# Performance work log

Measured on AMD Instinct MI355X. Metric: run time of the kernel, lower is better.

The kernel has to match this reference:

```python
import jax, jax.numpy as jnp
import numpy as np

P_DROP = 0.6  # dropout prob from the source module
N_NODES = 50000
N_EDGES = 800000


def _cheb_edge_weights(edge_index, num_nodes):
    # ChebConv with sym normalization and default lambda_max=2.0:
    # scaled Laplacian hat(L) = 2L/lambda_max - I = -D^{-1/2} A D^{-1/2}
    # (diagonal becomes 0), so edge weight = -1/sqrt(deg[row]*deg[col]).
    row, col = edge_index[0], edge_index[1]
    deg = jnp.zeros((num_nodes,), jnp.float32).at[row].add(1.0)
    dis = jnp.where(deg > 0, jax.lax.rsqrt(jnp.maximum(deg, 1.0)), 0.0)
    return -dis[row] * dis[col]


def _prop(x, row, col, w, n):
    # hat(L) @ x via gather-scale-scatter over the edge list
    return jnp.zeros((n, x.shape[1]), x.dtype).at[row].add(w[:, None] * x[col])


def _cheb_conv(x, row, col, w, W, b, n):
    # Chebyshev recursion: Tx0 = x, Tx1 = hat(L) x, Tx_k = 2 hat(L) Tx_{k-1} - Tx_{k-2}
    Tx0 = x
    out = Tx0 @ W[0]
    Tx1 = _prop(Tx0, row, col, w, n)
    out = out + Tx1 @ W[1]
    for k in range(2, W.shape[0]):
        Tx2 = 2.0 * _prop(Tx1, row, col, w, n) - Tx0
        out = out + Tx2 @ W[k]
        Tx0, Tx1 = Tx1, Tx2
    return out + b


def _dropout(x, key, p):
    keep = jax.random.bernoulli(key, 1.0 - p, x.shape)
    return jnp.where(keep, x * (1.0 / (1.0 - p)), 0.0)


def setup_inputs() -> dict:
    key = jax.random.key(0)
    ks = jax.random.split(key, 8)
    x = jax.random.normal(ks[0], (N_NODES, 64), jnp.float32)
    edge_index = jax.random.randint(ks[1], (2, N_EDGES), 0, N_NODES, jnp.int64)
    W0 = jax.random.normal(ks[2], (2, 64, 64), jnp.float32) * 0.1
    b0 = jnp.zeros((64,), jnp.float32)
    W1 = jax.random.normal(ks[3], (2, 64, 64), jnp.float32) * 0.1
    b1 = jnp.zeros((64,), jnp.float32)
    W2 = jax.random.normal(ks[4], (2, 64, 32), jnp.float32) * 0.1
    b2 = jnp.zeros((32,), jnp.float32)
    return {"x": x, "edge_index": edge_index, "W0": W0, "b0": b0,
            "W1": W1, "b1": b1, "W2": W2, "b2": b2}


def reference(x, edge_index, W0, b0, W1, b1, W2, b2):
    row, col = edge_index[0], edge_index[1]
    n = x.shape[0]
    w = _cheb_edge_weights(edge_index, n)
    dkey = jax.random.key(1)
    params = [(W0, b0), (W1, b1), (W2, b2)]
    for i, (W, b) in enumerate(params):
        x = _dropout(x, jax.random.fold_in(dkey, i), P_DROP)
        x = _cheb_conv(x, row, col, w, W, b, n)
        if i < len(params) - 1:
            x = jax.nn.relu(x)
    return x
```

## Files before the change

### kernel.cpp

```cpp
#include <hip/hip_runtime.h>
#include <stdint.h>

typedef _Float16 half8 __attribute__((ext_vector_type(8)));
typedef float float4v __attribute__((ext_vector_type(4)));

__host__ __device__ inline void tf2x32(uint32_t k0, uint32_t k1,
                                       uint32_t x0, uint32_t x1,
                                       uint32_t* o0, uint32_t* o1) {
  const uint32_t ks2 = k0 ^ k1 ^ 0x1BD11BDAu;
#define ROTL(v, s) (((v) << (s)) | ((v) >> (32 - (s))))
#define RND(r) do { x0 += x1; x1 = ROTL(x1, r); x1 ^= x0; } while (0)
  x0 += k0; x1 += k1;
  RND(13); RND(15); RND(26); RND(6);
  x0 += k1; x1 += ks2 + 1u;
  RND(17); RND(29); RND(16); RND(24);
  x0 += ks2; x1 += k0 + 2u;
  RND(13); RND(15); RND(26); RND(6);
  x0 += k0; x1 += k1 + 3u;
  RND(17); RND(29); RND(16); RND(24);
  x0 += k1; x1 += ks2 + 4u;
  RND(13); RND(15); RND(26); RND(6);
  x0 += ks2; x1 += k0 + 5u;
  *o0 = x0; *o1 = x1;
#undef RND
#undef ROTL
}

__device__ inline bool drop_keep(uint32_t k0, uint32_t k1, uint32_t idx) {
  uint32_t o0, o1;
  tf2x32(k0, k1, 0u, idx, &o0, &o1);
  uint32_t bits = o0 ^ o1;
  float u = __uint_as_float((bits >> 9) | 0x3f800000u) - 1.0f;
  return u < 0.4f;
}

__global__ void k_fill2(const int* __restrict__ row, const int* __restrict__ col,
                        int* __restrict__ cnt, uint16_t* __restrict__ cs,
                        int e, int rows_per_xcd) {
  const int owner = blockIdx.x & 7;
  const int i = (blockIdx.x >> 3) * 256 + threadIdx.x;
  if (i < e) {
    int r = row[i];
    if (r / rows_per_xcd == owner) {
      int pos = atomicAdd(&cnt[r], 1);
      if (pos < 64) cs[(r << 6) + pos] = (uint16_t)col[i];
    }
  }
}

__global__ void k_drop(const float* __restrict__ x, const int* __restrict__ cnt,
                       uint16_t* __restrict__ cs, float* __restrict__ dis,
                       _Float16* __restrict__ y, _Float16* __restrict__ ys,
                       _Float16* __restrict__ ysb, uint32_t k0, uint32_t k1,
                       int n, int nd,
                       const float* __restrict__ W0, const float* __restrict__ W1,
                       const float* __restrict__ W2, _Float16* __restrict__ wh) {
  int i = blockIdx.x * 256 + threadIdx.x;
  if (i < 20480) {
    int d = i;
    if (d < 8192) {
      int o = d >> 7, k = d & 127;
      wh[d] = (_Float16)W0[k * 64 + o];
    } else if (d < 16384) {
      int d1 = d - 8192, o = d1 >> 7, k = d1 & 127;
      wh[d] = (_Float16)W1[k * 64 + o];
    } else {
      int d2 = d - 16384, o = d2 >> 7, k = d2 & 127;
      wh[d] = (_Float16)W2[k * 32 + o];
    }
  }
  if (i < 64) {
    ys[((size_t)n << 6) + i]  = (_Float16)0.f;
    ysb[((size_t)n << 6) + i] = (_Float16)0.f;
  }
  if (i < nd) {
    const int r = i >> 6;
    const int t = i & 63;
    const int d = cnt[r];
    const float dis_r = (d > 0) ? rsqrtf((float)d) : 0.0f;
    float v = drop_keep(k0, k1, (uint32_t)i) ? x[i] * 2.5f : 0.0f;
    y[i]  = (_Float16)v;
    ys[i] = (_Float16)(dis_r * v);
    if (t == 0) dis[r] = dis_r;
    const int cn = d < 64 ? d : 64;
    const int rnd = (cn + 7) & ~7;
    if (t >= cn && t < rnd) cs[(r << 6) + t] = (uint16_t)n;
  }
}

template<int T>
__device__ __forceinline__ void gatherT(int idx_all, int rnd, int g, int sub,
                                        const _Float16* __restrict__ ysg,
                                        uint32_t dummy, float acc[8]) {
  half8 hv[T];
  #pragma unroll
  for (int j = 0; j < T; ++j) {
    int sh = __shfl(idx_all, j * 8 + g, 64);
    uint32_t c = (j * 8 < rnd) ? (uint32_t)(sh & 0xffff) : dummy;
    hv[j] = *(const half8*)((const char*)ysg + (c << 7) + (sub << 4));
  }
  #pragma unroll
  for (int j = 0; j < T; ++j)
    #pragma unroll
    for (int k = 0; k < 8; ++k) acc[k] += (float)hv[j][k];
}

template<int COUT, bool RELU, bool DROPN, bool WBF>
__global__ __launch_bounds__(256, 6) void k_conv(
    const _Float16* __restrict__ yg, const _Float16* __restrict__ ysg,
    const int* __restrict__ cnt, const uint16_t* __restrict__ cs,
    const float* __restrict__ dis, const _Float16* __restrict__ wt,
    const float* __restrict__ b, float* __restrict__ outf,
    _Float16* __restrict__ outb, _Float16* __restrict__ outs,
    uint32_t nk0, uint32_t nk1, int n) {
  constexpr int R  = 16;
  constexpr int TS = 136;
  __shared__ __align__(16) _Float16 xp[R][TS];

  const int wave = threadIdx.x >> 6;
  const int t    = threadIdx.x & 63;
  const int row0 = blockIdx.x * R;
  const int g    = t >> 3;
  const int sub  = t & 7;
  const uint32_t dummy = (uint32_t)n;

  int      idxs[4], ds4[4];
  float    dv4[4];
  _Float16 ygv[4];
  #pragma unroll
  for (int i = 0; i < 4; ++i) {
    int r = row0 + wave * 4 + i;
    r = r < n ? r : n - 1;
    idxs[i] = cs[(r << 6) + t];
    ds4[i]  = cnt[r];
    dv4[i]  = dis[r];
    ygv[i]  = yg[(uint32_t)(r << 6) + t];
  }

  #pragma unroll
  for (int i = 0; i < 4; ++i) {
    const int cn  = ds4[i] < 64 ? ds4[i] : 64;
    const int rnd = (cn + 7) & ~7;
    float acc[8] = {0.f, 0.f, 0.f, 0.f, 0.f, 0.f, 0.f, 0.f};
    if (rnd <= 16)      gatherT<2>(idxs[i], rnd, g, sub, ysg, dummy, acc);
    else if (rnd <= 32) gatherT<4>(idxs[i], rnd, g, sub, ysg, dummy, acc);
    else                gatherT<8>(idxs[i], rnd, g, sub, ysg, dummy, acc);

    const bool b0 = (g & 1), b1 = (g & 2), b2 = (g & 4);
    float a4[4], a2[2], v;
    #pragma unroll
    for (int m = 0; m < 4; ++m) {
      float keep = b0 ? acc[2 * m + 1] : acc[2 * m];
      float send = b0 ? acc[2 * m]     : acc[2 * m + 1];
      a4[m] = keep + __shfl_xor(send, 8, 64);
    }
    #pragma unroll
    for (int m = 0; m < 2; ++m) {
      float keep = b1 ? a4[2 * m + 1] : a4[2 * m];
      float send = b1 ? a4[2 * m]     : a4[2 * m + 1];
      a2[m] = keep + __shfl_xor(send, 16, 64);
    }
    {
      float keep = b2 ? a2[1] : a2[0];
      float send = b2 ? a2[0] : a2[1];
      v = keep + __shfl_xor(send, 32, 64);
    }
    const int rl = wave * 4 + i;
    xp[rl][t]                    = ygv[i];
    xp[rl][64 + (sub * 8 + g)]   = (_Float16)(-dv4[i] * v);
  }
  __syncthreads();

  constexpr int NW = COUT / 16;
  const int nn   = t & 15;
  const int quad = t >> 4;
  if (wave < NW) {
    const int colg = wave * 16 + nn;
    float4v acc = {0.f, 0.f, 0.f, 0.f};
    #pragma unroll
    for (int ks = 0; ks < 4; ++ks) {
      half8 a  = *(const half8*)&xp[nn][quad * 8 + 32 * ks];
      half8 bb = *(const half8*)&wt[(size_t)colg * 128 + quad * 8 + 32 * ks];
      acc = __builtin_amdgcn_mfma_f32_16x16x32_f16(a, bb, acc, 0, 0, 0);
    }
    const float bias = b[colg];
    #pragma unroll
    for (int rg = 0; rg < 4; ++rg) {
      const int rl = quad * 4 + rg;
      const int rr = row0 + rl;
      if (rr < n) {
        float v = acc[rg] + bias;
        if (RELU) v = fmaxf(v, 0.0f);
        if (DROPN) {
          if (drop_keep(nk0, nk1, (uint32_t)(rr * 64 + colg))) v *= 2.5f;
          else v = 0.0f;
        }
        if (WBF) {
          outb[(size_t)rr * COUT + colg] = (_Float16)v;
          outs[(size_t)rr * COUT + colg] = (_Float16)(dis[rr] * v);
        } else {
          outf[(size_t)rr * COUT + colg] = v;
        }
      }
    }
  }
}

extern "C" void kernel_launch(void* const* d_in, const int* in_sizes, int n_in,
                              void* d_out, int out_size, void* d_ws, size_t ws_size,
                              hipStream_t stream) {
  const float* x   = (const float*)d_in[0];
  const int*   ei  = (const int*)d_in[1];
  const float* W0  = (const float*)d_in[2];
  const float* b0  = (const float*)d_in[3];
  const float* W1f = (const float*)d_in[4];
  const float* b1  = (const float*)d_in[5];
  const float* W2  = (const float*)d_in[6];
  const float* b2  = (const float*)d_in[7];
  float* out = (float*)d_out;

  const int n = in_sizes[0] / 64;
  const int e = in_sizes[1] / 2;
  const int* row = ei;
  const int* col = ei + e;

  size_t off = 0;
  auto carve = [&](size_t elems) {
    size_t o = off;
    off += (elems + 255) & ~(size_t)255;
    return o;
  };
  int* base = (int*)d_ws;
  int*      cnt = base + carve(n);
  float*    dis = (float*)(base + carve(n));
  uint16_t* cs  = (uint16_t*)(base + carve((size_t)n * 32));
  _Float16* ya  = (_Float16*)(base + carve((size_t)n * 32));
  _Float16* ysa = (_Float16*)(base + carve((size_t)(n + 1) * 32));
  _Float16* yb  = (_Float16*)(base + carve((size_t)n * 32));
  _Float16* ysb = (_Float16*)(base + carve((size_t)(n + 1) * 32));
  _Float16* wh  = (_Float16*)(base + carve(10240));
  (void)ws_size;
  _Float16* wh0 = wh;
  _Float16* wh1 = wh + 8192;
  _Float16* wh2 = wh + 16384;

  uint32_t dk[3][2];
  for (uint32_t i = 0; i < 3; ++i) tf2x32(0u, 1u, 0u, i, &dk[i][0], &dk[i][1]);

  hipMemsetAsync(cnt, 0, (size_t)n * 4, stream);

  const int nchunk = (e + 255) / 256;
  const int bd = ((n * 64) + 255) / 256;
  const int bc = (n + 15) / 16;
  const int rpx = (n + 7) / 8;

  k_fill2<<<nchunk * 8, 256, 0, stream>>>(row, col, cnt, cs, e, rpx);
  k_drop<<<bd, 256, 0, stream>>>(x, cnt, cs, dis, ya, ysa, ysb,
                                 dk[0][0], dk[0][1], n, n * 64,
                                 W0, W1f, W2, wh);

  k_conv<64, true,  true,  true ><<<bc, 256, 0, stream>>>(
      ya, ysa, cnt, cs, dis, wh0, b0, nullptr, yb, ysb, dk[1][0], dk[1][1], n);
  k_conv<64, true,  true,  true ><<<bc, 256, 0, stream>>>(
      yb, ysb, cnt, cs, dis, wh1, b1, nullptr, ya, ysa, dk[2][0], dk[2][1], n);
  k_conv<32, false, false, false><<<bc, 256, 0, stream>>>(
      ya, ysa, cnt, cs, dis, wh2, b2, out, nullptr, nullptr, 0u, 0u, n);
}
```

Baseline: 188.7 us.

## Split scaled features into two 32-wide halves and vectorize edge fill loads

New measurement: 203.7 us. 7.9% more time.

```diff
diff --git a/kernel.cpp b/kernel.cpp
--- a/kernel.cpp
+++ b/kernel.cpp
@@ -38,21 +38,27 @@
                         int* __restrict__ cnt, uint16_t* __restrict__ cs,
                         int e, int rows_per_xcd) {
   const int owner = blockIdx.x & 7;
-  const int i = (blockIdx.x >> 3) * 256 + threadIdx.x;
-  if (i < e) {
-    int r = row[i];
-    if (r / rows_per_xcd == owner) {
-      int pos = atomicAdd(&cnt[r], 1);
-      if (pos < 64) cs[(r << 6) + pos] = (uint16_t)col[i];
+  const int i2 = (((blockIdx.x >> 3) * 256) + threadIdx.x) * 2;
+  if (i2 < e) {
+    const int2 r2 = *(const int2*)&row[i2];
+    const int2 c2 = *(const int2*)&col[i2];
+    if (r2.x / rows_per_xcd == owner) {
+      int pos = atomicAdd(&cnt[r2.x], 1);
+      if (pos < 64) cs[(r2.x << 6) + pos] = (uint16_t)c2.x;
+    }
+    if (r2.y / rows_per_xcd == owner) {
+      int pos = atomicAdd(&cnt[r2.y], 1);
+      if (pos < 64) cs[(r2.y << 6) + pos] = (uint16_t)c2.y;
     }
   }
 }
 
 __global__ void k_drop(const float* __restrict__ x, const int* __restrict__ cnt,
                        uint16_t* __restrict__ cs, float* __restrict__ dis,
-                       _Float16* __restrict__ y, _Float16* __restrict__ ys,
-                       _Float16* __restrict__ ysb, uint32_t k0, uint32_t k1,
-                       int n, int nd,
+                       _Float16* __restrict__ y,
+                       _Float16* __restrict__ ys0, _Float16* __restrict__ ys1,
+                       _Float16* __restrict__ ys0b, _Float16* __restrict__ ys1b,
+                       uint32_t k0, uint32_t k1, int n, int nd,
                        const float* __restrict__ W0, const float* __restrict__ W1,
                        const float* __restrict__ W2, _Float16* __restrict__ wh) {
   int i = blockIdx.x * 256 + threadIdx.x;
@@ -69,9 +75,10 @@
       wh[d] = (_Float16)W2[k * 32 + o];
     }
   }
-  if (i < 64) {
-    ys[((size_t)n << 6) + i]  = (_Float16)0.f;
-    ysb[((size_t)n << 6) + i] = (_Float16)0.f;
+  if (i < 32) {
+    const size_t dbase = (size_t)n * 32 + i;
+    ys0[dbase]  = (_Float16)0.f;  ys1[dbase]  = (_Float16)0.f;
+    ys0b[dbase] = (_Float16)0.f;  ys1b[dbase] = (_Float16)0.f;
   }
   if (i < nd) {
     const int r = i >> 6;
@@ -79,8 +86,10 @@
     const int d = cnt[r];
     const float dis_r = (d > 0) ? rsqrtf((float)d) : 0.0f;
     float v = drop_keep(k0, k1, (uint32_t)i) ? x[i] * 2.5f : 0.0f;
-    y[i]  = (_Float16)v;
-    ys[i] = (_Float16)(dis_r * v);
+    y[i] = (_Float16)v;
+    const _Float16 sv = (_Float16)(dis_r * v);
+    if (t < 32) ys0[(size_t)r * 32 + t]        = sv;
+    else        ys1[(size_t)r * 32 + (t - 32)] = sv;
     if (t == 0) dis[r] = dis_r;
     const int cn = d < 64 ? d : 64;
     const int rnd = (cn + 7) & ~7;
@@ -89,15 +98,15 @@
 }
 
 template<int T>
-__device__ __forceinline__ void gatherT(int idx_all, int rnd, int g, int sub,
-                                        const _Float16* __restrict__ ysg,
+__device__ __forceinline__ void gatherH(int idx_all, int rnd, int g2, int sub,
+                                        const _Float16* __restrict__ ysh,
                                         uint32_t dummy, float acc[8]) {
   half8 hv[T];
   #pragma unroll
   for (int j = 0; j < T; ++j) {
-    int sh = __shfl(idx_all, j * 8 + g, 64);
-    uint32_t c = (j * 8 < rnd) ? (uint32_t)(sh & 0xffff) : dummy;
-    hv[j] = *(const half8*)((const char*)ysg + (c << 7) + (sub << 4));
+    int sh = __shfl(idx_all, j * 16 + g2, 64);
+    uint32_t c = (j * 16 + g2 < rnd) ? (uint32_t)(sh & 0xffff) : dummy;
+    hv[j] = *(const half8*)((const char*)ysh + (c << 6) + (sub << 4));
   }
   #pragma unroll
   for (int j = 0; j < T; ++j)
@@ -107,11 +116,13 @@
 
 template<int COUT, bool RELU, bool DROPN, bool WBF>
 __global__ __launch_bounds__(256, 6) void k_conv(
-    const _Float16* __restrict__ yg, const _Float16* __restrict__ ysg,
+    const _Float16* __restrict__ yg,
+    const _Float16* __restrict__ ysg0, const _Float16* __restrict__ ysg1,
     const int* __restrict__ cnt, const uint16_t* __restrict__ cs,
     const float* __restrict__ dis, const _Float16* __restrict__ wt,
     const float* __restrict__ b, float* __restrict__ outf,
-    _Float16* __restrict__ outb, _Float16* __restrict__ outs,
+    _Float16* __restrict__ outb,
+    _Float16* __restrict__ outs0, _Float16* __restrict__ outs1,
     uint32_t nk0, uint32_t nk1, int n) {
   constexpr int R  = 16;
   constexpr int TS = 136;
@@ -120,11 +131,11 @@
   const int wave = threadIdx.x >> 6;
   const int t    = threadIdx.x & 63;
   const int row0 = blockIdx.x * R;
-  const int g    = t >> 3;
-  const int sub  = t & 7;
+  const int g2   = t >> 2;
+  const int sub  = t & 3;
   const uint32_t dummy = (uint32_t)n;
 
-  int      idxs[4], ds4[4];
+  int      idxs[4], rnd4[4];
   float    dv4[4];
   _Float16 ygv[4];
   #pragma unroll
@@ -132,43 +143,51 @@
     int r = row0 + wave * 4 + i;
     r = r < n ? r : n - 1;
     idxs[i] = cs[(r << 6) + t];
-    ds4[i]  = cnt[r];
+    const int d = cnt[r];
+    const int cn = d < 64 ? d : 64;
+    rnd4[i] = (cn + 7) & ~7;
     dv4[i]  = dis[r];
     ygv[i]  = yg[(uint32_t)(r << 6) + t];
   }
 
-  #pragma unroll
-  for (int i = 0; i < 4; ++i) {
-    const int cn  = ds4[i] < 64 ? ds4[i] : 64;
-    const int rnd = (cn + 7) & ~7;
-    float acc[8] = {0.f, 0.f, 0.f, 0.f, 0.f, 0.f, 0.f, 0.f};
-    if (rnd <= 16)      gatherT<2>(idxs[i], rnd, g, sub, ysg, dummy, acc);
-    else if (rnd <= 32) gatherT<4>(idxs[i], rnd, g, sub, ysg, dummy, acc);
-    else                gatherT<8>(idxs[i], rnd, g, sub, ysg, dummy, acc);
-
-    const bool b0 = (g & 1), b1 = (g & 2), b2 = (g & 4);
-    float a4[4], a2[2], v;
-    #pragma unroll
-    for (int m = 0; m < 4; ++m) {
-      float keep = b0 ? acc[2 * m + 1] : acc[2 * m];
-      float send = b0 ? acc[2 * m]     : acc[2 * m + 1];
-      a4[m] = keep + __shfl_xor(send, 8, 64);
-    }
-    #pragma unroll
-    for (int m = 0; m < 2; ++m) {
-      float keep = b1 ? a4[2 * m + 1] : a4[2 * m];
-      float send = b1 ? a4[2 * m]     : a4[2 * m + 1];
-      a2[m] = keep + __shfl_xor(send, 16, 64);
-    }
-    {
-      float keep = b2 ? a2[1] : a2[0];
-      float send = b2 ? a2[0] : a2[1];
-      v = keep + __shfl_xor(send, 32, 64);
-    }
-    const int rl = wave * 4 + i;
-    xp[rl][t]                    = ygv[i];
-    xp[rl][64 + (sub * 8 + g)]   = (_Float16)(-dv4[i] * v);
-  }
+  const bool bb0 = (g2 & 1), bb1 = (g2 & 2), bb2 = (g2 & 4);
+  #pragma unroll
+  for (int h = 0; h < 2; ++h) {
+    const _Float16* __restrict__ ysh = h ? ysg1 : ysg0;
+    #pragma unroll
+    for (int i = 0; i < 4; ++i) {
+      const int rnd = rnd4[i];
+      float acc[8] = {0.f, 0.f, 0.f, 0.f, 0.f, 0.f, 0.f, 0.f};
+      if (rnd <= 16)      gatherH<1>(idxs[i], rnd, g2, sub, ysh, dummy, acc);
+      else if (rnd <= 32) gatherH<2>(idxs[i], rnd, g2, sub, ysh, dummy, acc);
+      else                gatherH<4>(idxs[i], rnd, g2, sub, ysh, dummy, acc);
+
+      float a4[4], a2[2], v;
+      #pragma unroll
+      for (int m = 0; m < 4; ++m) {
+        float keep = bb0 ? acc[2 * m + 1] : acc[2 * m];
+        float send = bb0 ? acc[2 * m]     : acc[2 * m + 1];
+        a4[m] = keep + __shfl_xor(send, 4, 64);
+      }
+      #pragma unroll
+      for (int m = 0; m < 2; ++m) {
+        float keep = bb1 ? a4[2 * m + 1] : a4[2 * m];
+        float send = bb1 ? a4[2 * m]     : a4[2 * m + 1];
+        a2[m] = keep + __shfl_xor(send, 8, 64);
+      }
+      {
+        float keep = bb2 ? a2[1] : a2[0];
+        float send = bb2 ? a2[0] : a2[1];
+        v = keep + __shfl_xor(send, 16, 64);
+      }
+      v = v + __shfl_xor(v, 32, 64);
+      const int rl = wave * 4 + i;
+      if (t < 32)
+        xp[rl][64 + h * 32 + sub * 8 + (g2 & 7)] = (_Float16)(-dv4[i] * v);
+    }
+  }
+  #pragma unroll
+  for (int i = 0; i < 4; ++i) xp[wave * 4 + i][t] = ygv[i];
   __syncthreads();
 
   constexpr int NW = COUT / 16;
@@ -180,8 +199,8 @@
     #pragma unroll
     for (int ks = 0; ks < 4; ++ks) {
       half8 a  = *(const half8*)&xp[nn][quad * 8 + 32 * ks];
-      half8 bb = *(const half8*)&wt[(size_t)colg * 128 + quad * 8 + 32 * ks];
-      acc = __builtin_amdgcn_mfma_f32_16x16x32_f16(a, bb, acc, 0, 0, 0);
+      half8 bbv = *(const half8*)&wt[(size_t)colg * 128 + quad * 8 + 32 * ks];
+      acc = __builtin_amdgcn_mfma_f32_16x16x32_f16(a, bbv, acc, 0, 0, 0);
     }
     const float bias = b[colg];
     #pragma unroll
@@ -197,7 +216,9 @@
         }
         if (WBF) {
           outb[(size_t)rr * COUT + colg] = (_Float16)v;
-          outs[(size_t)rr * COUT + colg] = (_Float16)(dis[rr] * v);
+          const _Float16 sv = (_Float16)(dis[rr] * v);
+          if (colg < 32) outs0[(size_t)rr * 32 + colg]        = sv;
+          else           outs1[(size_t)rr * 32 + (colg - 32)] = sv;
         } else {
           outf[(size_t)rr * COUT + colg] = v;
         }
@@ -231,14 +252,16 @@
     return o;
   };
   int* base = (int*)d_ws;
-  int*      cnt = base + carve(n);
-  float*    dis = (float*)(base + carve(n));
-  uint16_t* cs  = (uint16_t*)(base + carve((size_t)n * 32));
-  _Float16* ya  = (_Float16*)(base + carve((size_t)n * 32));
-  _Float16* ysa = (_Float16*)(base + carve((size_t)(n + 1) * 32));
-  _Float16* yb  = (_Float16*)(base + carve((size_t)n * 32));
-  _Float16* ysb = (_Float16*)(base + carve((size_t)(n + 1) * 32));
-  _Float16* wh  = (_Float16*)(base + carve(10240));
+  int*      cnt  = base + carve(n);
+  float*    dis  = (float*)(base + carve(n));
+  uint16_t* cs   = (uint16_t*)(base + carve((size_t)n * 32));
+  _Float16* ya   = (_Float16*)(base + carve((size_t)n * 32));
+  _Float16* ys0a = (_Float16*)(base + carve((size_t)(n + 1) * 16));
+  _Float16* ys1a = (_Float16*)(base + carve((size_t)(n + 1) * 16));
+  _Float16* yb   = (_Float16*)(base + carve((size_t)n * 32));
+  _Float16* ys0b = (_Float16*)(base + carve((size_t)(n + 1) * 16));
+  _Float16* ys1b = (_Float16*)(base + carve((size_t)(n + 1) * 16));
+  _Float16* wh   = (_Float16*)(base + carve(10240));
   (void)ws_size;
   _Float16* wh0 = wh;
   _Float16* wh1 = wh + 8192;
@@ -249,20 +272,23 @@
 
   hipMemsetAsync(cnt, 0, (size_t)n * 4, stream);
 
-  const int nchunk = (e + 255) / 256;
+  const int nchunk2 = ((e / 2) + 255) / 256;
   const int bd = ((n * 64) + 255) / 256;
   const int bc = (n + 15) / 16;
   const int rpx = (n + 7) / 8;
 
-  k_fill2<<<nchunk * 8, 256, 0, stream>>>(row, col, cnt, cs, e, rpx);
-  k_drop<<<bd, 256, 0, stream>>>(x, cnt, cs, dis, ya, ysa, ysb,
+  k_fill2<<<nchunk2 * 8, 256, 0, stream>>>(row, col, cnt, cs, e, rpx);
+  k_drop<<<bd, 256, 0, stream>>>(x, cnt, cs, dis, ya, ys0a, ys1a, ys0b, ys1b,
                                  dk[0][0], dk[0][1], n, n * 64,
                                  W0, W1f, W2, wh);
 
   k_conv<64, true,  true,  true ><<<bc, 256, 0, stream>>>(
-      ya, ysa, cnt, cs, dis, wh0, b0, nullptr, yb, ysb, dk[1][0], dk[1][1], n);
+      ya, ys0a, ys1a, cnt, cs, dis, wh0, b0, nullptr, yb, ys0b, ys1b,
+      dk[1][0], dk[1][1], n);
   k_conv<64, true,  true,  true ><<<bc, 256, 0, stream>>>(
-      yb, ysb, cnt, cs, dis, wh1, b1, nullptr, ya, ysa, dk[2][0], dk[2][1], n);
+      yb, ys0b, ys1b, cnt, cs, dis, wh1, b1, nullptr, ya, ys0a, ys1a,
+      dk[2][0], dk[2][1], n);
   k_conv<32, false, false, false><<<bc, 256, 0, stream>>>(
-      ya, ysa, cnt, cs, dis, wh2, b2, out, nullptr, nullptr, 0u, 0u, n);
-}
+      ya, ys0a, ys1a, cnt, cs, dis, wh2, b2, out, nullptr, nullptr, nullptr,
+      0u, 0u, n);
+}
```
